# Performance work log

Measured on AMD Instinct MI355X. Metric: run time of the kernel, lower is better.

The kernel has to match this reference:

```python
import jax, jax.numpy as jnp
import numpy as np

B, HH, WW, E = 8, 128, 128, 192
NH = 8
D1 = (3 * E) // NH * NH  # 576
HD = D1 // NH            # 72
RPE = 512
LAYERS = 3
EPS = 1e-8


def srms(x):
    # SimpleRMSNorm: x / (||x||_2 / sqrt(d) + eps), no learned params
    d = x.shape[-1]
    norm = jnp.linalg.norm(x, axis=-1, keepdims=True)
    return x / (norm * (d ** -0.5) + EPS)


def rpe_net(idx, pos_w, pos_b, lw, lb, out_w, out_b):
    # idx: (L, 1) float positions -> (NH, L, HD) Toeplitz coefficients
    h = idx @ pos_w.T + pos_b  # (L, RPE)
    for i in range(LAYERS):   # residual=False
        h = jax.nn.relu(srms(h)) @ lw[i].T + lb[i]
    h = jax.nn.relu(srms(h)) @ out_w.T + out_b  # (L, NH*HD)
    return h.reshape(idx.shape[0], NH, HD).transpose(1, 0, 2)


def tno(v, axis, pos_w, pos_b, lw, lb, out_w, out_b):
    # v: (b, h, H, W, d); Toeplitz mixing along `axis` (-3 or -2), non-causal,
    # par_type=1, no decay, act_type='none', normalize=False.
    n = v.shape[axis]
    z = jnp.zeros((1,), jnp.float32)
    p = jnp.arange(1, n, dtype=jnp.float32)
    # coefficient layout for length-2n circular conv: a0, a1..a(n-1), a0, a-(n-1)..a-1
    idx = jnp.concatenate([z, p, z, -p[::-1]]).reshape(-1, 1)  # (2n, 1)
    a = rpe_net(idx, pos_w, pos_b, lw, lb, out_w, out_b)       # (NH, 2n, HD)
    ak = a[:, None, :, :] if axis == -2 else a[:, :, None, :]
    y = jnp.fft.rfft(v, 2 * n, axis=axis)
    af = jnp.fft.rfft(ak, 2 * n, axis=axis)
    out = jnp.fft.irfft(af * y, 2 * n, axis=axis)
    return out[..., :n, :] if axis == -2 else out[..., :n, :, :]


def setup_inputs() -> dict:
    key = jax.random.key(0)
    ks = jax.random.split(key, 19)
    s = 0.02
    rn = lambda k, shape, sc=s: jax.random.normal(k, shape, dtype=jnp.float32) * sc
    inp = {
        'x': jax.random.normal(ks[0], (B, HH, WW, E), dtype=jnp.float32),
        'u_w': rn(ks[1], (D1, E)), 'u_b': rn(ks[2], (D1,)),
        'v_w': rn(ks[3], (D1, E)), 'v_b': rn(ks[4], (D1,)),
        'o_w': rn(ks[5], (E, D1)), 'o_b': rn(ks[6], (E,)),
    }
    for i, name in enumerate(['rpe1', 'rpe2']):
        off = 7 + i * 6
        inp[name + '_pos_w'] = rn(ks[off], (RPE, 1), 0.5)
        inp[name + '_pos_b'] = rn(ks[off + 1], (RPE,), 0.5)
        inp[name + '_lw'] = rn(ks[off + 2], (LAYERS, RPE, RPE))
        inp[name + '_lb'] = rn(ks[off + 3], (LAYERS, RPE))
        inp[name + '_out_w'] = rn(ks[off + 4], (NH * HD, RPE))
        inp[name + '_out_b'] = rn(ks[off + 5], (NH * HD,))
    inp['H'] = HH
    inp['W'] = WW
    return inp


def reference(x, u_w, u_b, v_w, v_b, o_w, o_b,
              rpe1_pos_w, rpe1_pos_b, rpe1_lw, rpe1_lb, rpe1_out_w, rpe1_out_b,
              rpe2_pos_w, rpe2_pos_b, rpe2_lw, rpe2_lb, rpe2_out_w, rpe2_out_b,
              H, W):
    shortcut = x
    xn = srms(x)                              # pre_norm (SimpleRMSNorm)
    u = jax.nn.silu(xn @ u_w.T + u_b)         # (B,H,W,D1)
    v = jax.nn.silu(xn @ v_w.T + v_b)
    b = v.shape[0]
    v = v.reshape(b, H, W, NH, HD).transpose(0, 3, 1, 2, 4)  # b h H W d
    out = (tno(v, -3, rpe2_pos_w, rpe2_pos_b, rpe2_lw, rpe2_lb, rpe2_out_w, rpe2_out_b)
           + tno(v, -2, rpe1_pos_w, rpe1_pos_b, rpe1_lw, rpe1_lb, rpe1_out_w, rpe1_out_b))
    out = out.transpose(0, 2, 3, 1, 4).reshape(b, H, W, NH * HD)  # b H W (h d)
    out = u * out
    return out @ o_w.T + o_b + shortcut
```

## Files before the change

### kernel.cpp

```cpp
#include <hip/hip_runtime.h>
#include <hip/hip_bf16.h>

typedef __hip_bfloat16 bf16;
typedef __attribute__((ext_vector_type(4))) float f32x4;
typedef __attribute__((ext_vector_type(8))) __bf16 bf16x8;
typedef __attribute__((ext_vector_type(4))) __bf16 bf16x4;

constexpr int NB  = 8;
constexpr int NHH = 128;
constexpr int NWW = 128;
constexpr int NE  = 192;
constexpr int ND  = 576;
constexpr int NR  = 512;
constexpr int NL  = 256;
constexpr int NP  = NB * NHH * NWW;
constexpr int NPC = NHH * NWW;

__device__ __forceinline__ void gload16(const void* g, void* l) {
    __builtin_amdgcn_global_load_lds(
        (const __attribute__((address_space(1))) unsigned int*)g,
        (__attribute__((address_space(3))) unsigned int*)l, 16, 0, 0);
}

__global__ void k_rpe_pos(const float* __restrict__ pw1, const float* __restrict__ pb1,
                          const float* __restrict__ pw2, const float* __restrict__ pb2,
                          float* __restrict__ h)
{
    int net = blockIdx.x >> 8;
    int l   = blockIdx.x & 255;
    const float* pw = net ? pw2 : pw1;
    const float* pb = net ? pb2 : pb1;
    float idxv;
    if (l == 0 || l == 128) idxv = 0.f;
    else if (l < 128)       idxv = (float)l;
    else                    idxv = (float)(l - 256);
    float* hr = h + ((size_t)net * NL + l) * NR;
    for (int r = threadIdx.x; r < NR; r += 256)
        hr[r] = idxv * pw[r] + pb[r];
}

__global__ __launch_bounds__(256) void k_wt(
    const float* __restrict__ lw1, const float* __restrict__ ow1,
    const float* __restrict__ lw2, const float* __restrict__ ow2,
    float* __restrict__ wt)
{
    __shared__ float tile[32][33];
    int m = blockIdx.z, net = m >> 2, sub = m & 3;
    int J = (sub == 3) ? 576 : 512;
    const float* src = (sub == 3) ? (net ? ow2 : ow1)
                                  : (net ? lw2 : lw1) + (size_t)sub * 262144;
    float* dst = wt + (size_t)net * 1081344 + ((sub == 3) ? 786432 : sub * 262144);
    int r0 = blockIdx.x * 32, j0 = blockIdx.y * 32;
    if (j0 >= J) return;
    int tx = threadIdx.x, ty = threadIdx.y;
    #pragma unroll
    for (int d = 0; d < 4; ++d) {
        int j = j0 + ty + d * 8;
        tile[ty + d * 8][tx] = (j < J) ? src[(size_t)j * 512 + r0 + tx] : 0.f;
    }
    __syncthreads();
    #pragma unroll
    for (int d = 0; d < 4; ++d) {
        int r = r0 + ty + d * 8;
        int j = j0 + tx;
        if (j < J) dst[(size_t)r * J + j] = tile[tx][ty + d * 8];
    }
}

__global__ __launch_bounds__(256) void k_rpe_layer(
    const float* __restrict__ hin,
    const float* __restrict__ Wt1, const float* __restrict__ b1,
    const float* __restrict__ Wt2, const float* __restrict__ b2,
    float* __restrict__ out1, float* __restrict__ out2, int outdim)
{
    __shared__ float g[2][NR];
    __shared__ float red[256];
    int net = blockIdx.x >> 7;
    int l0  = (blockIdx.x & 127) * 2;
    const float* hr = hin + ((size_t)net * NL + l0) * NR;
    int tid = threadIdx.x;
    int row = tid >> 7, ix = tid & 127;
    const float* hh = hr + (size_t)row * NR;
    float a0 = hh[ix], a1 = hh[ix + 128], a2 = hh[ix + 256], a3 = hh[ix + 384];
    red[tid] = a0 * a0 + a1 * a1 + a2 * a2 + a3 * a3;
    __syncthreads();
    for (int off = 64; off; off >>= 1) {
        if (ix < off) red[tid] += red[tid + off];
        __syncthreads();
    }
    float sc = 1.f / (sqrtf(red[row << 7]) * 0.044194173824159216f + 1e-8f);
    g[row][ix]       = fmaxf(a0 * sc, 0.f);
    g[row][ix + 128] = fmaxf(a1 * sc, 0.f);
    g[row][ix + 256] = fmaxf(a2 * sc, 0.f);
    g[row][ix + 384] = fmaxf(a3 * sc, 0.f);
    __syncthreads();
    const float* Wt = net ? Wt2 : Wt1;
    const float* bb = net ? b2 : b1;
    float* o0 = (net ? out2 : out1) + (size_t)l0 * outdim;
    int half = outdim >> 1;
    for (int jj = tid; jj < half; jj += 256) {
        float ax0 = 0.f, ay0 = 0.f, ax1 = 0.f, ay1 = 0.f;
        const float* wp = Wt + 2 * jj;
        #pragma unroll 8
        for (int r = 0; r < NR; ++r) {
            float2 w = *(const float2*)(wp + (size_t)r * outdim);
            float g0 = g[0][r], g1 = g[1][r];
            ax0 = fmaf(g0, w.x, ax0); ay0 = fmaf(g0, w.y, ay0);
            ax1 = fmaf(g1, w.x, ax1); ay1 = fmaf(g1, w.y, ay1);
        }
        float bx = bb[2 * jj], by = bb[2 * jj + 1];
        o0[2 * jj]              = ax0 + bx;  o0[2 * jj + 1]          = ay0 + by;
        o0[outdim + 2 * jj]     = ax1 + bx;  o0[outdim + 2 * jj + 1] = ay1 + by;
    }
}

__global__ __launch_bounds__(256) void k_toep(
    const float* __restrict__ A1, const float* __restrict__ A2, bf16* __restrict__ T)
{
    __shared__ float Als[256][17];
    int cb = blockIdx.x, rq = blockIdx.y, net = blockIdx.z;
    const float* A = net ? A2 : A1;
    int tid = threadIdx.x;
    #pragma unroll
    for (int i = 0; i < 16; ++i) {
        int el = i * 256 + tid;
        int k = el >> 4, cl = el & 15;
        Als[k][cl] = A[(size_t)k * ND + cb * 16 + cl];
    }
    __syncthreads();
    int cl = tid >> 4, sg = tid & 15;
    __bf16* Tb = (__bf16*)T + (((size_t)net * ND + cb * 16 + cl) * 128) * 128;
    for (int rr = 0; rr < 32; ++rr) {
        int r = rq * 32 + rr;
        bf16x8 o;
        #pragma unroll
        for (int j = 0; j < 8; ++j) {
            int s = sg * 8 + j;
            o[j] = (__bf16)Als[(r - s) & 255][cl];
        }
        *(bf16x8*)(Tb + (size_t)r * 128 + sg * 8) = o;
    }
}

__global__ void k_scale(const float* __restrict__ x, float* __restrict__ scl)
{
    int wave = (blockIdx.x * blockDim.x + threadIdx.x) >> 6;
    int lane = threadIdx.x & 63;
    int nw   = (gridDim.x * blockDim.x) >> 6;
    for (int p = wave; p < NP; p += nw) {
        const float* xp = x + (size_t)p * NE;
        float v0 = xp[lane], v1 = xp[lane + 64], v2 = xp[lane + 128];
        float ss = v0 * v0 + v1 * v1 + v2 * v2;
        for (int off = 32; off; off >>= 1) ss += __shfl_xor(ss, off, 64);
        if (lane == 0)
            scl[p] = 1.0f / (sqrtf(ss) * 0.07216878364870323f + 1e-8f);
    }
}

__global__ void k_wconv(const float* __restrict__ uw, const float* __restrict__ vw,
                        const float* __restrict__ ow,
                        bf16* __restrict__ wb, bf16* __restrict__ owb)
{
    int i = blockIdx.x * 256 + threadIdx.x;
    constexpr int S = ND * NE;
    if (i < S)          wb[i]  = __float2bfloat16(uw[i]);
    else if (i < 2 * S) wb[i]  = __float2bfloat16(vw[i - S]);
    else                owb[i - 2 * S] = __float2bfloat16(ow[i - 2 * S]);
}

__global__ __launch_bounds__(256) void k_uv(
    const float* __restrict__ x, const float* __restrict__ scl,
    const bf16* __restrict__ wb,
    const float* __restrict__ ub, const float* __restrict__ vb,
    bf16* __restrict__ u_t, bf16* __restrict__ v_t)
{
    __shared__ __align__(16) char smem[33792];
    __bf16 (*sA)[64] = (__bf16(*)[64])smem;
    __bf16 (*sB)[64] = (__bf16(*)[64])(smem + 16384);
    __bf16* ldst = (__bf16*)smem;
    int tid = threadIdx.x;
    int wv = tid >> 6, lane = tid & 63;
    int b = blockIdx.x;
    int chunk = b & 7;
    int s = b >> 3;
    int by = s / 9;
    int ntile = s - by * 9;
    int nbase = ntile * 128;
    int wr = wv >> 1, wc = wv & 1;
    int lrow = lane >> 3, lcol = lane & 7;
    int ar = tid >> 1, ah = tid & 1;
    size_t prow = (size_t)chunk * NPC + by * 128 + ar;
    float ascl = scl[prow];
    const float* xrow = x + prow * NE;
    f32x4 acc[4][4] = {};
    for (int kk = 0; kk < 3; ++kk) {
        {
            const float4* xp = (const float4*)(xrow + kk * 64 + ah * 32);
            #pragma unroll
            for (int i = 0; i < 4; ++i) {
                float4 f0 = xp[2 * i], f1 = xp[2 * i + 1];
                bf16x8 o;
                o[0] = (__bf16)(f0.x * ascl); o[1] = (__bf16)(f0.y * ascl);
                o[2] = (__bf16)(f0.z * ascl); o[3] = (__bf16)(f0.w * ascl);
                o[4] = (__bf16)(f1.x * ascl); o[5] = (__bf16)(f1.y * ascl);
                o[6] = (__bf16)(f1.z * ascl); o[7] = (__bf16)(f1.w * ascl);
                *(bf16x8*)&sA[ar][ah * 32 + i * 8] = o;
            }
        }
        #pragma unroll
        for (int i = 0; i < 4; ++i) {
            int row = wv * 32 + i * 8;
            gload16((const char*)(wb + (size_t)(nbase + row + lrow) * NE + kk * 64) + lcol * 16,
                    &sB[row][0]);
        }
        asm volatile("s_waitcnt vmcnt(0)" ::: "memory");
        __syncthreads();
        #pragma unroll
        for (int k2 = 0; k2 < 2; ++k2) {
            bf16x8 af[4], bw[4];
            #pragma unroll
            for (int m = 0; m < 4; ++m)
                af[m] = *(const bf16x8*)&sA[wr * 64 + m * 16 + (lane & 15)][k2 * 32 + (lane >> 4) * 8];
            #pragma unroll
            for (int n = 0; n < 4; ++n)
                bw[n] = *(const bf16x8*)&sB[wc * 64 + n * 16 + (lane & 15)][k2 * 32 + (lane >> 4) * 8];
            #pragma unroll
            for (int m = 0; m < 4; ++m)
                #pragma unroll
                for (int n = 0; n < 4; ++n)
                    acc[m][n] = __builtin_amdgcn_mfma_f32_16x16x32_bf16(af[m], bw[n], acc[m][n], 0, 0, 0);
        }
        __syncthreads();
    }
    int fr = lane & 15, fq = lane >> 4;
    #pragma unroll
    for (int m = 0; m < 4; ++m) {
        #pragma unroll
        for (int n = 0; n < 4; ++n) {
            int jn_l = wc * 64 + n * 16 + fr;
            int jn_g = nbase + jn_l;
            float bias = (jn_g < ND) ? ub[jn_g] : vb[jn_g - ND];
            bf16x4 val;
            #pragma unroll
            for (int j = 0; j < 4; ++j) {
                float z = acc[m][n][j] + bias;
                float sgl = z / (1.f + __expf(-z));
                val[j] = (__bf16)sgl;
            }
            *(bf16x4*)&ldst[jn_l * 132 + wr * 64 + m * 16 + fq * 4] = val;
        }
    }
    __syncthreads();
    size_t pgl = (size_t)chunk * NPC + (size_t)by * 128 + (tid & 15) * 8;
    #pragma unroll
    for (int pass = 0; pass < 8; ++pass) {
        int row = (tid >> 4) + pass * 16;
        int jn_g = nbase + row;
        int colb = (tid & 15) * 8;
        bf16x4 a = *(bf16x4*)&ldst[row * 132 + colb];
        bf16x4 bb = *(bf16x4*)&ldst[row * 132 + colb + 4];
        bf16x8 o;
        #pragma unroll
        for (int i = 0; i < 4; ++i) { o[i] = a[i]; o[i + 4] = bb[i]; }
        __bf16* dst = (jn_g < ND) ? (__bf16*)u_t + (size_t)jn_g * NP + pgl
                                  : (__bf16*)v_t + (size_t)(jn_g - ND) * NP + pgl;
        *(bf16x8*)dst = o;
    }
}

__global__ __launch_bounds__(256) void k_conv(
    bf16* __restrict__ v_t, const bf16* __restrict__ T, const bf16* __restrict__ u_t)
{
    __shared__ __bf16 Vp[128][132];
    int tid = threadIdx.x;
    int b = blockIdx.x;
    int c = (b & 7) * 72 + ((b >> 3) >> 3);
    int chunk = (b >> 3) & 7;
    size_t pbase = (size_t)c * NP + (size_t)chunk * NPC;
    const __bf16* vsrc = (const __bf16*)v_t + pbase;
    #pragma unroll
    for (int it = 0; it < 8; ++it) {
        int y = (tid >> 4) + 16 * it;
        int x0 = (tid & 15) * 8;
        bf16x8 rd = *(const bf16x8*)(vsrc + (size_t)y * 128 + x0);
        bf16x4 lo, hi;
        #pragma unroll
        for (int i = 0; i < 4; ++i) { lo[i] = rd[i]; hi[i] = rd[i + 4]; }
        *(bf16x4*)&Vp[y][x0]     = lo;
        *(bf16x4*)&Vp[y][x0 + 4] = hi;
    }
    __syncthreads();
    int wv = tid >> 6, lane = tid & 63;
    int wr = wv >> 1, wc = wv & 1;
    int fr = lane & 15, q = lane >> 4;
    const __bf16* T1 = (const __bf16*)T + (size_t)c * 16384;
    const __bf16* T2 = (const __bf16*)T + (size_t)(ND + c) * 16384;
    f32x4 acc[4][4] = {};
    #pragma unroll
    for (int k = 0; k < 4; ++k) {
        bf16x8 af[4], bw[4];
        #pragma unroll
        for (int m = 0; m < 4; ++m) {
            int row = wr * 64 + m * 16 + fr;
            bf16x4 a = *(const bf16x4*)&Vp[row][k * 32 + q * 8];
            bf16x4 bb = *(const bf16x4*)&Vp[row][k * 32 + q * 8 + 4];
            #pragma unroll
            for (int i = 0; i < 4; ++i) { af[m][i] = a[i]; af[m][i + 4] = bb[i]; }
        }
        #pragma unroll
        for (int n = 0; n < 4; ++n)
            bw[n] = *(const bf16x8*)(T1 + (size_t)(wc * 64 + n * 16 + fr) * 128 + k * 32 + q * 8);
        #pragma unroll
        for (int m = 0; m < 4; ++m)
            #pragma unroll
            for (int n = 0; n < 4; ++n)
                acc[m][n] = __builtin_amdgcn_mfma_f32_16x16x32_bf16(af[m], bw[n], acc[m][n], 0, 0, 0);
    }
    #pragma unroll
    for (int k = 0; k < 4; ++k) {
        bf16x8 a2[4], b2[4];
        #pragma unroll
        for (int m = 0; m < 4; ++m)
            a2[m] = *(const bf16x8*)(T2 + (size_t)(wr * 64 + m * 16 + fr) * 128 + k * 32 + q * 8);
        #pragma unroll
        for (int n = 0; n < 4; ++n) {
            int xc = wc * 64 + n * 16 + fr;
            #pragma unroll
            for (int j = 0; j < 8; ++j)
                b2[n][j] = Vp[k * 32 + q * 8 + j][xc];
        }
        #pragma unroll
        for (int m = 0; m < 4; ++m)
            #pragma unroll
            for (int n = 0; n < 4; ++n)
                acc[m][n] = __builtin_amdgcn_mfma_f32_16x16x32_bf16(a2[m], b2[n], acc[m][n], 0, 0, 0);
    }
    __syncthreads();
    #pragma unroll
    for (int m = 0; m < 4; ++m) {
        #pragma unroll
        for (int n = 0; n < 4; ++n) {
            int xc = wc * 64 + n * 16 + fr;
            #pragma unroll
            for (int j = 0; j < 4; ++j) {
                int y = wr * 64 + m * 16 + q * 4 + j;
                Vp[y][xc] = (__bf16)acc[m][n][j];
            }
        }
    }
    __syncthreads();
    const __bf16* usrc = (const __bf16*)u_t + pbase;
    __bf16* vdst = (__bf16*)v_t + pbase;
    #pragma unroll
    for (int it = 0; it < 8; ++it) {
        int y = (tid >> 4) + 16 * it;
        int x0 = (tid & 15) * 8;
        bf16x8 uu = *(const bf16x8*)(usrc + (size_t)y * 128 + x0);
        bf16x4 lo = *(const bf16x4*)&Vp[y][x0];
        bf16x4 hi = *(const bf16x4*)&Vp[y][x0 + 4];
        bf16x8 o;
        #pragma unroll
        for (int i = 0; i < 4; ++i) {
            o[i]     = (__bf16)((float)uu[i]     * (float)lo[i]);
            o[i + 4] = (__bf16)((float)uu[i + 4] * (float)hi[i]);
        }
        *(bf16x8*)(vdst + (size_t)y * 128 + x0) = o;
    }
}

__global__ __launch_bounds__(256) void k_out(
    const bf16* __restrict__ g_t, const bf16* __restrict__ owb,
    const float* __restrict__ ob, const float* __restrict__ x, float* __restrict__ out)
{
    __shared__ __bf16 gs[64][132];
    int tid = threadIdx.x;
    int pt = blockIdx.x;
    int wv = tid >> 6, lane = tid & 63;
    int wr = wv >> 1, wc = wv & 1;
    int fr = lane & 15, q = lane >> 4;
    f32x4 acc[4][6] = {};
    for (int kk = 0; kk < 9; ++kk) {
        #pragma unroll
        for (int i = 0; i < 4; ++i) {
            int cl = (tid >> 4) + 16 * i;
            int pg = (tid & 15) * 8;
            bf16x8 rd = *(const bf16x8*)((const __bf16*)g_t + (size_t)(kk * 64 + cl) * NP
                                         + (size_t)pt * 128 + pg);
            bf16x4 lo, hi;
            #pragma unroll
            for (int ii = 0; ii < 4; ++ii) { lo[ii] = rd[ii]; hi[ii] = rd[ii + 4]; }
            *(bf16x4*)&gs[cl][pg]     = lo;
            *(bf16x4*)&gs[cl][pg + 4] = hi;
        }
        __syncthreads();
        #pragma unroll
        for (int ks = 0; ks < 2; ++ks) {
            bf16x8 af[4], bw[6];
            #pragma unroll
            for (int m = 0; m < 4; ++m) {
                int prow = wr * 64 + m * 16 + fr;
                #pragma unroll
                for (int j = 0; j < 8; ++j)
                    af[m][j] = gs[ks * 32 + q * 8 + j][prow];
            }
            #pragma unroll
            for (int n = 0; n < 6; ++n) {
                int e = wc * 96 + n * 16 + fr;
                bw[n] = *(const bf16x8*)((const __bf16*)owb + (size_t)e * ND + kk * 64 + ks * 32 + q * 8);
            }
            #pragma unroll
            for (int m = 0; m < 4; ++m)
                #pragma unroll
                for (int n = 0; n < 6; ++n)
                    acc[m][n] = __builtin_amdgcn_mfma_f32_16x16x32_bf16(af[m], bw[n], acc[m][n], 0, 0, 0);
        }
        __syncthreads();
    }
    #pragma unroll
    for (int m = 0; m < 4; ++m) {
        #pragma unroll
        for (int n = 0; n < 6; ++n) {
            int e = wc * 96 + n * 16 + fr;
            float bias = ob[e];
            #pragma unroll
            for (int j = 0; j < 4; ++j) {
                size_t p = (size_t)pt * 128 + wr * 64 + m * 16 + q * 4 + j;
                out[p * NE + e] = acc[m][n][j] + bias + x[p * NE + e];
            }
        }
    }
}

extern "C" void kernel_launch(void* const* d_in, const int* in_sizes, int n_in,
                              void* d_out, int out_size, void* d_ws, size_t ws_size,
                              hipStream_t stream)
{
    const float* x    = (const float*)d_in[0];
    const float* u_w  = (const float*)d_in[1];
    const float* u_b  = (const float*)d_in[2];
    const float* v_w  = (const float*)d_in[3];
    const float* v_b  = (const float*)d_in[4];
    const float* o_w  = (const float*)d_in[5];
    const float* o_b  = (const float*)d_in[6];
    const float* r1_pw = (const float*)d_in[7];
    const float* r1_pb = (const float*)d_in[8];
    const float* r1_lw = (const float*)d_in[9];
    const float* r1_lb = (const float*)d_in[10];
    const float* r1_ow = (const float*)d_in[11];
    const float* r1_ob = (const float*)d_in[12];
    const float* r2_pw = (const float*)d_in[13];
    const float* r2_pb = (const float*)d_in[14];
    const float* r2_lw = (const float*)d_in[15];
    const float* r2_lb = (const float*)d_in[16];
    const float* r2_ow = (const float*)d_in[17];
    const float* r2_ob = (const float*)d_in[18];
    float* out = (float*)d_out;

    float* A1 = (float*)d_ws;
    float* A2 = A1 + (size_t)NL * ND;
    float* h0 = A2 + (size_t)NL * ND;
    float* h1 = h0 + (size_t)2 * NL * NR;
    float* wt = h1 + (size_t)2 * NL * NR;
    float* scl = wt + (size_t)2 * 1081344;
    bf16* T   = (bf16*)(scl + NP);
    bf16* u_t = T + (size_t)2 * ND * NPC;
    bf16* v_t = u_t + (size_t)ND * NP;
    bf16* wb  = v_t + (size_t)ND * NP;
    bf16* owb = wb + (size_t)2 * ND * NE;

    k_rpe_pos<<<dim3(512), dim3(256), 0, stream>>>(r1_pw, r1_pb, r2_pw, r2_pb, h0);
    k_wt<<<dim3(16, 18, 8), dim3(32, 8), 0, stream>>>(r1_lw, r1_ow, r2_lw, r2_ow, wt);
    {
        const float* src[3] = { h0, h1, h0 };
        float* dst[3]       = { h1, h0, h1 };
        for (int i = 0; i < 3; ++i) {
            k_rpe_layer<<<dim3(256), dim3(256), 0, stream>>>(
                src[i], wt + (size_t)i * 262144, r1_lb + (size_t)i * NR,
                        wt + 1081344 + (size_t)i * 262144, r2_lb + (size_t)i * NR,
                dst[i], dst[i] + (size_t)NL * NR, NR);
        }
        k_rpe_layer<<<dim3(256), dim3(256), 0, stream>>>(
            h1, wt + 786432, r1_ob, wt + 1081344 + 786432, r2_ob, A1, A2, ND);
    }
    k_toep<<<dim3(36, 4, 2), dim3(256), 0, stream>>>(A1, A2, T);
    k_wconv<<<dim3(1296), dim3(256), 0, stream>>>(u_w, v_w, o_w, wb, owb);
    k_scale<<<dim3(2048), dim3(256), 0, stream>>>(x, scl);

    k_uv<<<dim3(9216), dim3(256), 0, stream>>>(x, scl, wb, u_b, v_b, u_t, v_t);
    k_conv<<<dim3(4608), dim3(256), 0, stream>>>(v_t, T, u_t);
    k_out<<<dim3(1024), dim3(256), 0, stream>>>(v_t, owb, o_b, x, out);
}
```

Measured before the change: 634.0 us.

## Pre-normalize x to swizzled bf16 and stream both GEMM operands via LDS DMA

Adds a k_prep kernel that scales x by its RMS factor once and writes a bf16 copy in an XOR-swizzled layout. The weight conversion writes the same swizzled layout and now converts eight elements per thread. k_uv then loads both A and B tiles with global_load_lds and reads LDS through the swizzle to avoid bank conflicts. This removes the x fp32 re-read and conversion that each of the 9 N-tiles repeated. The cost is an extra pass over x, a bf16 buffer of x in the workspace, and a workspace reshuffle where T now aliases h0.

```diff
diff --git a/kernel.cpp b/kernel.cpp
--- a/kernel.cpp
+++ b/kernel.cpp
@@ -157,20 +157,51 @@
     }
 }
 
+__global__ void k_prep(const float* __restrict__ x, const float* __restrict__ scl,
+                       bf16* __restrict__ xbn)
+{
+    int gid = blockIdx.x * 256 + threadIdx.x;
+    int p = gid / 24, bb = gid - p * 24;
+    float sc = scl[p];
+    const float4* src = (const float4*)(x + (size_t)p * NE + bb * 8);
+    float4 f0 = src[0], f1 = src[1];
+    bf16x8 o;
+    o[0] = (__bf16)(f0.x * sc); o[1] = (__bf16)(f0.y * sc);
+    o[2] = (__bf16)(f0.z * sc); o[3] = (__bf16)(f0.w * sc);
+    o[4] = (__bf16)(f1.x * sc); o[5] = (__bf16)(f1.y * sc);
+    o[6] = (__bf16)(f1.z * sc); o[7] = (__bf16)(f1.w * sc);
+    int t = (bb & 24) | ((bb & 7) ^ (p & 7));
+    *(bf16x8*)((__bf16*)xbn + (size_t)p * NE + t * 8) = o;
+}
+
 __global__ void k_wconv(const float* __restrict__ uw, const float* __restrict__ vw,
                         const float* __restrict__ ow,
                         bf16* __restrict__ wb, bf16* __restrict__ owb)
 {
-    int i = blockIdx.x * 256 + threadIdx.x;
-    constexpr int S = ND * NE;
-    if (i < S)          wb[i]  = __float2bfloat16(uw[i]);
-    else if (i < 2 * S) wb[i]  = __float2bfloat16(vw[i - S]);
-    else                owb[i - 2 * S] = __float2bfloat16(ow[i - 2 * S]);
+    int gid = blockIdx.x * 256 + threadIdx.x;
+    if (gid < 27648) {
+        int row = gid / 24, bb = gid - row * 24;
+        const float* src = ((row < ND) ? uw + (size_t)row * NE
+                                       : vw + (size_t)(row - ND) * NE) + bb * 8;
+        float4 f0 = ((const float4*)src)[0], f1 = ((const float4*)src)[1];
+        bf16x8 o;
+        o[0] = (__bf16)f0.x; o[1] = (__bf16)f0.y; o[2] = (__bf16)f0.z; o[3] = (__bf16)f0.w;
+        o[4] = (__bf16)f1.x; o[5] = (__bf16)f1.y; o[6] = (__bf16)f1.z; o[7] = (__bf16)f1.w;
+        int t = (bb & 24) | ((bb & 7) ^ (row & 7));
+        *(bf16x8*)((__bf16*)wb + (size_t)row * NE + t * 8) = o;
+    } else if (gid < 27648 + 13824) {
+        int g = gid - 27648;
+        const float* src = ow + (size_t)g * 8;
+        float4 f0 = ((const float4*)src)[0], f1 = ((const float4*)src)[1];
+        bf16x8 o;
+        o[0] = (__bf16)f0.x; o[1] = (__bf16)f0.y; o[2] = (__bf16)f0.z; o[3] = (__bf16)f0.w;
+        o[4] = (__bf16)f1.x; o[5] = (__bf16)f1.y; o[6] = (__bf16)f1.z; o[7] = (__bf16)f1.w;
+        *(bf16x8*)((__bf16*)owb + (size_t)g * 8) = o;
+    }
 }
 
 __global__ __launch_bounds__(256) void k_uv(
-    const float* __restrict__ x, const float* __restrict__ scl,
-    const bf16* __restrict__ wb,
+    const bf16* __restrict__ xbn, const bf16* __restrict__ wb,
     const float* __restrict__ ub, const float* __restrict__ vb,
     bf16* __restrict__ u_t, bf16* __restrict__ v_t)
 {
@@ -188,42 +219,33 @@
     int nbase = ntile * 128;
     int wr = wv >> 1, wc = wv & 1;
     int lrow = lane >> 3, lcol = lane & 7;
-    int ar = tid >> 1, ah = tid & 1;
-    size_t prow = (size_t)chunk * NPC + by * 128 + ar;
-    float ascl = scl[prow];
-    const float* xrow = x + prow * NE;
+    size_t gbase = (size_t)chunk * NPC + by * 128;
     f32x4 acc[4][4] = {};
     for (int kk = 0; kk < 3; ++kk) {
-        {
-            const float4* xp = (const float4*)(xrow + kk * 64 + ah * 32);
-            #pragma unroll
-            for (int i = 0; i < 4; ++i) {
-                float4 f0 = xp[2 * i], f1 = xp[2 * i + 1];
-                bf16x8 o;
-                o[0] = (__bf16)(f0.x * ascl); o[1] = (__bf16)(f0.y * ascl);
-                o[2] = (__bf16)(f0.z * ascl); o[3] = (__bf16)(f0.w * ascl);
-                o[4] = (__bf16)(f1.x * ascl); o[5] = (__bf16)(f1.y * ascl);
-                o[6] = (__bf16)(f1.z * ascl); o[7] = (__bf16)(f1.w * ascl);
-                *(bf16x8*)&sA[ar][ah * 32 + i * 8] = o;
-            }
-        }
         #pragma unroll
         for (int i = 0; i < 4; ++i) {
             int row = wv * 32 + i * 8;
+            gload16((const char*)(xbn + (gbase + row + lrow) * NE + kk * 64) + lcol * 16,
+                    &sA[row][0]);
             gload16((const char*)(wb + (size_t)(nbase + row + lrow) * NE + kk * 64) + lcol * 16,
                     &sB[row][0]);
         }
         asm volatile("s_waitcnt vmcnt(0)" ::: "memory");
         __syncthreads();
+        int q = lane >> 4, fr = lane & 15;
         #pragma unroll
         for (int k2 = 0; k2 < 2; ++k2) {
             bf16x8 af[4], bw[4];
             #pragma unroll
-            for (int m = 0; m < 4; ++m)
-                af[m] = *(const bf16x8*)&sA[wr * 64 + m * 16 + (lane & 15)][k2 * 32 + (lane >> 4) * 8];
-            #pragma unroll
-            for (int n = 0; n < 4; ++n)
-                bw[n] = *(const bf16x8*)&sB[wc * 64 + n * 16 + (lane & 15)][k2 * 32 + (lane >> 4) * 8];
+            for (int m = 0; m < 4; ++m) {
+                int frm = wr * 64 + m * 16 + fr;
+                af[m] = *(const bf16x8*)&sA[frm][(((k2 << 2) | q) ^ (frm & 7)) * 8];
+            }
+            #pragma unroll
+            for (int n = 0; n < 4; ++n) {
+                int fn = wc * 64 + n * 16 + fr;
+                bw[n] = *(const bf16x8*)&sB[fn][(((k2 << 2) | q) ^ (fn & 7)) * 8];
+            }
             #pragma unroll
             for (int m = 0; m < 4; ++m)
                 #pragma unroll
@@ -251,7 +273,7 @@
         }
     }
     __syncthreads();
-    size_t pgl = (size_t)chunk * NPC + (size_t)by * 128 + (tid & 15) * 8;
+    size_t pgl = gbase + (tid & 15) * 8;
     #pragma unroll
     for (int pass = 0; pass < 8; ++pass) {
         int row = (tid >> 4) + pass * 16;
@@ -456,17 +478,18 @@
     const float* r2_ob = (const float*)d_in[18];
     float* out = (float*)d_out;
 
-    float* A1 = (float*)d_ws;
-    float* A2 = A1 + (size_t)NL * ND;
-    float* h0 = A2 + (size_t)NL * ND;
+    float* A1  = (float*)d_ws;
+    float* A2  = A1 + (size_t)NL * ND;
+    float* scl = A2 + (size_t)NL * ND;
+    bf16* wb   = (bf16*)(scl + NP);
+    bf16* owb  = wb + (size_t)2 * ND * NE;
+    bf16* u_t  = owb + (size_t)NE * ND;
+    bf16* v_t  = u_t + (size_t)ND * NP;
+    bf16* xbn  = v_t + (size_t)ND * NP;
+    float* h0 = (float*)(xbn + (size_t)NP * NE);
     float* h1 = h0 + (size_t)2 * NL * NR;
     float* wt = h1 + (size_t)2 * NL * NR;
-    float* scl = wt + (size_t)2 * 1081344;
-    bf16* T   = (bf16*)(scl + NP);
-    bf16* u_t = T + (size_t)2 * ND * NPC;
-    bf16* v_t = u_t + (size_t)ND * NP;
-    bf16* wb  = v_t + (size_t)ND * NP;
-    bf16* owb = wb + (size_t)2 * ND * NE;
+    bf16* T   = (bf16*)h0;
 
     k_rpe_pos<<<dim3(512), dim3(256), 0, stream>>>(r1_pw, r1_pb, r2_pw, r2_pb, h0);
     k_wt<<<dim3(16, 18, 8), dim3(32, 8), 0, stream>>>(r1_lw, r1_ow, r2_lw, r2_ow, wt);
@@ -483,10 +506,11 @@
             h1, wt + 786432, r1_ob, wt + 1081344 + 786432, r2_ob, A1, A2, ND);
     }
     k_toep<<<dim3(36, 4, 2), dim3(256), 0, stream>>>(A1, A2, T);
-    k_wconv<<<dim3(1296), dim3(256), 0, stream>>>(u_w, v_w, o_w, wb, owb);
+    k_wconv<<<dim3(162), dim3(256), 0, stream>>>(u_w, v_w, o_w, wb, owb);
     k_scale<<<dim3(2048), dim3(256), 0, stream>>>(x, scl);
-
-    k_uv<<<dim3(9216), dim3(256), 0, stream>>>(x, scl, wb, u_b, v_b, u_t, v_t);
+    k_prep<<<dim3(12288), dim3(256), 0, stream>>>(x, scl, xbn);
+
+    k_uv<<<dim3(9216), dim3(256), 0, stream>>>(xbn, wb, u_b, v_b, u_t, v_t);
     k_conv<<<dim3(4608), dim3(256), 0, stream>>>(v_t, T, u_t);
     k_out<<<dim3(1024), dim3(256), 0, stream>>>(v_t, owb, o_b, x, out);
 }
```

After: 596.9 us. 1.06x faster.
